# Performance work log

Hardware: AMD Instinct MI355X
Metric: run time of the kernel (lower is better)

The kernel has to match this reference:

```python
import jax, jax.numpy as jnp
import numpy as np

N_NODES = 100000
N_EDGES = 1200000
IN_FEATS = 64
OUT_FEATS = 64


def setup_inputs() -> dict:
    key = jax.random.key(0)
    k1, k2, k3, k4 = jax.random.split(key, 4)
    feature = jax.random.normal(k1, (N_NODES, IN_FEATS), dtype=jnp.float32)
    edge_src = jax.random.randint(k2, (N_EDGES,), 0, N_NODES, dtype=jnp.int32)
    edge_dst = jax.random.randint(k3, (N_EDGES,), 0, N_NODES, dtype=jnp.int32)
    # xavier_normal_ init for linear weight (fan_in=fan_out=64)
    std = float(np.sqrt(2.0 / (IN_FEATS + OUT_FEATS)))
    W = jax.random.normal(k4, (OUT_FEATS, IN_FEATS), dtype=jnp.float32) * std
    b = jnp.zeros((OUT_FEATS,), dtype=jnp.float32)
    return {"feature": feature, "edge_src": edge_src, "edge_dst": edge_dst, "W": W, "b": b}


def reference(feature, edge_src, edge_dst, W, b):
    # copy_src: gather source-node features per edge, then mean-reduce by dst.
    msgs = feature[edge_src]                                   # [E, d_in]
    summed = jax.ops.segment_sum(msgs, edge_dst, num_segments=N_NODES)  # [N, d_in]
    deg = jax.ops.segment_sum(jnp.ones((edge_src.shape[0],), feature.dtype),
                              edge_dst, num_segments=N_NODES)  # [N]
    h = summed / jnp.maximum(deg, 1.0)[:, None]                # mean; 0 for isolated nodes
    # apply_nodes: linear + activation
    h = jnp.einsum("nd,od->no", h, W) + b
    return jax.nn.relu(h)
```

## Files before the change

### kernel.cpp

```cpp
#include <hip/hip_runtime.h>


typedef __attribute__((ext_vector_type(8))) short short8;
typedef __attribute__((ext_vector_type(4))) float floatx4;

constexpr int kNodes = 100000;
constexpr int kEdges = 1200000;

constexpr int kBuckets = 2048;
constexpr int kBucketNodes = 49;

constexpr int kBinBlocks = 256;
constexpr int kEdgesPerBlock = 4688;
constexpr int kEPT = (kEdgesPerBlock + 1023) / 1024;

constexpr int kCap = 1024;
constexpr float kFxScale = 262144.0f;
constexpr int kAccStride = 68;

constexpr int kWsFeat   = 0;
constexpr int kWsOff    = 3200000;
constexpr int kWsBinned = kWsOff + (kBuckets + 1) * kBinBlocks;

__device__ __forceinline__ unsigned bf16rne(float f) {
  unsigned u = __float_as_uint(f);
  return (u + 0x7fffu + ((u >> 16) & 1u)) >> 16;
}

__global__ __launch_bounds__(1024) void gcn_build(
    const float* __restrict__ feat,
    const int* __restrict__ src, const int* __restrict__ dst,
    int* __restrict__ ws) {
  uint4* fb16 = (uint4*)(ws + kWsFeat);
  int* offTT  = ws + kWsOff;
  int* binned = ws + kWsBinned;

  __shared__ int lhist[kBuckets];
  __shared__ int lcur[kBuckets];
  __shared__ int wsum[16];

  const int tid = threadIdx.x;
  lhist[tid] = 0;
  lhist[tid + 1024] = 0;
  __syncthreads();

  const int e0 = blockIdx.x * kEdgesPerBlock;
  const int cnt = min(kEdgesPerBlock, kEdges - e0);
  int es[kEPT], ebk[kEPT], edl[kEPT];
  #pragma unroll
  for (int k = 0; k < kEPT; ++k) {
    const int j = tid + k * 1024;
    if (j < cnt) {
      es[k] = src[e0 + j];
      const int d = dst[e0 + j];
      const int bk = d / kBucketNodes;
      ebk[k] = bk;
      edl[k] = d - bk * kBucketNodes;
      atomicAdd(&lhist[bk], 1);
    }
  }

  const int t = blockIdx.x * 1024 + tid;
  for (int i = t; i < kNodes * 8; i += kBinBlocks * 1024) {
    const float* fr = feat + (size_t)(i >> 3) * 64 + (i & 7);
    uint4 p;
    p.x = bf16rne(fr[0])  | (bf16rne(fr[8])  << 16);
    p.y = bf16rne(fr[16]) | (bf16rne(fr[24]) << 16);
    p.z = bf16rne(fr[32]) | (bf16rne(fr[40]) << 16);
    p.w = bf16rne(fr[48]) | (bf16rne(fr[56]) << 16);
    fb16[i] = p;
  }
  __syncthreads();

  const int a  = lhist[tid * 2];
  const int b2 = lhist[tid * 2 + 1];
  const int own = a + b2;
  const int wv = tid >> 6, ln = tid & 63;
  int sc = own;
  #pragma unroll
  for (int off = 1; off < 64; off <<= 1) {
    const int v = __shfl_up(sc, off, 64);
    if (ln >= off) sc += v;
  }
  if (ln == 63) wsum[wv] = sc;
  __syncthreads();
  if (tid < 64) {
    int tw = (tid < 16) ? wsum[tid] : 0;
    #pragma unroll
    for (int off = 1; off < 16; off <<= 1) {
      const int v = __shfl_up(tw, off, 64);
      if (tid >= off) tw += v;
    }
    if (tid < 16) wsum[tid] = tw;
  }
  __syncthreads();
  const int e0p = sc - own + (wv ? wsum[wv - 1] : 0);
  lcur[tid * 2]     = e0p;
  lcur[tid * 2 + 1] = e0p + a;
  offTT[(tid * 2) * kBinBlocks + blockIdx.x]     = e0p;
  offTT[(tid * 2 + 1) * kBinBlocks + blockIdx.x] = e0p + a;
  if (tid == 0) offTT[kBuckets * kBinBlocks + blockIdx.x] = cnt;
  __syncthreads();

  int* myBin = binned + blockIdx.x * kEdgesPerBlock;
  #pragma unroll
  for (int k = 0; k < kEPT; ++k) {
    const int j = tid + k * 1024;
    if (j < cnt) {
      const int pos = atomicAdd(&lcur[ebk[k]], 1);
      myBin[pos] = es[k] | (edl[k] << 17);
    }
  }
}

__global__ __launch_bounds__(512, 8) void gcn_aggregate(
    const int*   __restrict__ ws_in,
    const float* __restrict__ W,
    const float* __restrict__ b,
    float*       __restrict__ out) {
  const uint4* fb16 = (const uint4*)(ws_in + kWsFeat);
  const int* offTT  = ws_in + kWsOff;
  const int* binned = ws_in + kWsBinned;

  __shared__ __align__(16) char uShared[64 * 72 * 2];
  __shared__ __align__(16) int accum[kBucketNodes * kAccStride];
  __shared__ int    deg[64];
  __shared__ int    sh[64];
  __shared__ int    runL[kBinBlocks + 1];
  __shared__ int    runG[kBinBlocks];
  __shared__ ushort Wb16[64 * 64];
  __shared__ float  bsh[64];
  int*    lsrc  = (int*)uShared;
  ushort* hsAll = (ushort*)uShared;

  const int tid = threadIdx.x;
  const int bkt = blockIdx.x;

  if (tid < 64) { deg[tid] = 0; sh[tid] = 0; bsh[tid] = b[tid]; }
  for (int i = tid; i < 4096; i += 512) Wb16[i] = (ushort)bf16rne(W[i]);
  for (int i = tid; i < kBucketNodes * kAccStride; i += 512) accum[i] = 0;

  if (tid < kBinBlocks) {
    const int o0 = offTT[bkt * kBinBlocks + tid];
    const int o1 = offTT[(bkt + 1) * kBinBlocks + tid];
    runL[tid] = o1 - o0;
    runG[tid] = tid * kEdgesPerBlock + o0;
  }
  __syncthreads();
  if (tid < 64) {
    const int base = tid * 4;
    const int v0 = runL[base], v1 = runL[base + 1];
    const int v2 = runL[base + 2], v3 = runL[base + 3];
    const int p1 = v0 + v1, p2 = p1 + v2, tot = p2 + v3;
    int sc = tot;
    #pragma unroll
    for (int off = 1; off < 64; off <<= 1) {
      const int v = __shfl_up(sc, off, 64);
      if (tid >= off) sc += v;
    }
    const int ex = sc - tot;
    runL[base]     = ex;
    runL[base + 1] = ex + v0;
    runL[base + 2] = ex + p1;
    runL[base + 3] = ex + p2;
    if (tid == 63) runL[kBinBlocks] = sc;
  }
  __syncthreads();

  int sz = runL[kBinBlocks];
  if (sz > kCap) sz = kCap;

  auto mapRead = [&](int j) -> unsigned {
    int lo = 0, hi = kBinBlocks;
    #pragma unroll
    for (int it = 0; it < 8; ++it) {
      const int mid = (lo + hi) >> 1;
      if (runL[mid] <= j) lo = mid; else hi = mid;
    }
    return (unsigned)binned[runG[lo] + (j - runL[lo])];
  };

  const int j0 = tid, j1 = tid + 512;
  const bool va = j0 < sz, vb = j1 < sz;
  unsigned ea = 0, eb = 0;
  if (va) {
    ea = mapRead(j0);
    atomicAdd(&deg[ea >> 17], 1);
    atomicAdd(&sh[(ea & 0x1FFFFu) >> 11], 1);
  }
  if (vb) {
    eb = mapRead(j1);
    atomicAdd(&deg[eb >> 17], 1);
    atomicAdd(&sh[(eb & 0x1FFFFu) >> 11], 1);
  }
  __syncthreads();

  if (tid < 64) {
    const int own = sh[tid];
    int s = own;
    #pragma unroll
    for (int off = 1; off < 64; off <<= 1) {
      const int v = __shfl_up(s, off, 64);
      if (tid >= off) s += v;
    }
    sh[tid] = s - own;
  }
  __syncthreads();

  if (va) { const int p = atomicAdd(&sh[(ea & 0x1FFFFu) >> 11], 1); lsrc[p] = (int)ea; }
  if (vb) { const int p = atomicAdd(&sh[(eb & 0x1FFFFu) >> 11], 1); lsrc[p] = (int)eb; }
  __syncthreads();

  const int wave = tid >> 6;
  const int lane = tid & 63;
  const int g = lane >> 3;
  const int c = lane & 7;
  {
    const int slot = wave * 8 + g;
    #pragma unroll 2
    for (int j = slot; j < sz; j += 64) {
      const unsigned e = (unsigned)lsrc[j];
      const uint4 v = fb16[(size_t)(e & 0x1FFFFu) * 8 + c];
      int* rp = accum + (int)(e >> 17) * kAccStride + c;
      atomicAdd(rp + 0,  (int)(__uint_as_float(v.x << 16)          * kFxScale));
      atomicAdd(rp + 8,  (int)(__uint_as_float(v.x & 0xffff0000u) * kFxScale));
      atomicAdd(rp + 16, (int)(__uint_as_float(v.y << 16)          * kFxScale));
      atomicAdd(rp + 24, (int)(__uint_as_float(v.y & 0xffff0000u) * kFxScale));
      atomicAdd(rp + 32, (int)(__uint_as_float(v.z << 16)          * kFxScale));
      atomicAdd(rp + 40, (int)(__uint_as_float(v.z & 0xffff0000u) * kFxScale));
      atomicAdd(rp + 48, (int)(__uint_as_float(v.w << 16)          * kFxScale));
      atomicAdd(rp + 56, (int)(__uint_as_float(v.w & 0xffff0000u) * kFxScale));
    }
  }
  __syncthreads();

  {
    const int nd = tid >> 3;
    const int ch = tid & 7;
    if (nd < kBucketNodes) {
      const int dg = deg[nd];
      const float inv = 1.0f / (kFxScale * (float)(dg > 1 ? dg : 1));
      const int* arow = accum + nd * kAccStride + ch * 8;
      const int4 pa = *(const int4*)(arow);
      const int4 pb = *(const int4*)(arow + 4);
      unsigned h0 = bf16rne((float)pa.x * inv);
      unsigned h1 = bf16rne((float)pa.y * inv);
      unsigned h2 = bf16rne((float)pa.z * inv);
      unsigned h3 = bf16rne((float)pa.w * inv);
      unsigned h4 = bf16rne((float)pb.x * inv);
      unsigned h5 = bf16rne((float)pb.y * inv);
      unsigned h6 = bf16rne((float)pb.z * inv);
      unsigned h7 = bf16rne((float)pb.w * inv);
      uint4 pk;
      pk.x = h0 | (h1 << 16);
      pk.y = h2 | (h3 << 16);
      pk.z = h4 | (h5 << 16);
      pk.w = h6 | (h7 << 16);
      *(uint4*)(hsAll + nd * 72 + ch * 8) = pk;
    } else {
      *(uint4*)(hsAll + nd * 72 + ch * 8) = make_uint4(0u, 0u, 0u, 0u);
    }
  }
  __syncthreads();

  if (tid < 256) {
    const int w8   = tid >> 6;
    const int ln   = tid & 63;
    const int quad = ln >> 4;
    const int col  = ln & 15;
    const int n0 = bkt * kBucketNodes;

    const short8 af0 = *reinterpret_cast<const short8*>(
        hsAll + (w8 * 16 + col) * 72 + 0 * 32 + quad * 8);
    const short8 af1 = *reinterpret_cast<const short8*>(
        hsAll + (w8 * 16 + col) * 72 + 1 * 32 + quad * 8);

    #pragma unroll
    for (int ob = 0; ob < 4; ++ob) {
      const short8 bf0 = *reinterpret_cast<const short8*>(
          Wb16 + (ob * 16 + col) * 64 + 0 * 32 + quad * 8);
      const short8 bf1 = *reinterpret_cast<const short8*>(
          Wb16 + (ob * 16 + col) * 64 + 1 * 32 + quad * 8);
      floatx4 acc = {0.f, 0.f, 0.f, 0.f};
      acc = __builtin_amdgcn_mfma_f32_16x16x32_bf16(af0, bf0, acc, 0, 0, 0);
      acc = __builtin_amdgcn_mfma_f32_16x16x32_bf16(af1, bf1, acc, 0, 0, 0);

      const int o = ob * 16 + col;
      const float bo = bsh[o];
      #pragma unroll
      for (int r = 0; r < 4; ++r) {
        const int local = w8 * 16 + quad * 4 + r;
        const int node = n0 + local;
        if (local < kBucketNodes && node < kNodes) {
          const float v = acc[r] + bo;
          out[(size_t)node * 64 + o] = v > 0.0f ? v : 0.0f;
        }
      }
    }
  }
}

extern "C" void kernel_launch(void* const* d_in, const int* in_sizes, int n_in,
                              void* d_out, int out_size, void* d_ws, size_t ws_size,
                              hipStream_t stream) {
  const float* feature  = (const float*)d_in[0];
  const int*   edge_src = (const int*)  d_in[1];
  const int*   edge_dst = (const int*)  d_in[2];
  const float* W        = (const float*)d_in[3];
  const float* b        = (const float*)d_in[4];

  float* out = (float*)d_out;
  int*   ws  = (int*)d_ws;

  gcn_build<<<kBinBlocks, 1024, 0, stream>>>(feature, edge_src, edge_dst, ws);
  gcn_aggregate<<<kBuckets, 512, 0, stream>>>(ws, W, b, out);
}
```

Baseline: 131.4 us.

## Replace two-level binned edge sort with global atomic bucket append

Drops the per-block histogram, scan and offset table. Each edge now claims a slot in its fixed-capacity bucket region through a global atomicAdd, and the W-to-bf16 conversion moves into a small prep kernel that also zeroes the counters. The aggregate kernel reads its bucket's edges directly instead of binary-searching 256 runs, and reads W and b from global memory instead of staging them in shared memory. In exchange it adds global atomic contention on 2048 counters and lowers the per-bucket cap to 768, so any edges past the cap are silently dropped.

New measurement: 261.9 us. +99.2%, slower.

```diff
diff --git a/kernel.cpp b/kernel.cpp
--- a/kernel.cpp
+++ b/kernel.cpp
@@ -10,58 +10,42 @@
 constexpr int kBuckets = 2048;
 constexpr int kBucketNodes = 49;
 
-constexpr int kBinBlocks = 256;
-constexpr int kEdgesPerBlock = 4688;
-constexpr int kEPT = (kEdgesPerBlock + 1023) / 1024;
-
-constexpr int kCap = 1024;
+constexpr int kCap = 768;
 constexpr float kFxScale = 262144.0f;
 constexpr int kAccStride = 68;
 
 constexpr int kWsFeat   = 0;
-constexpr int kWsOff    = 3200000;
-constexpr int kWsBinned = kWsOff + (kBuckets + 1) * kBinBlocks;
+constexpr int kWsCnt    = 3200000;
+constexpr int kWsWb     = 3202048;
+constexpr int kWsSorted = 3204096;
 
 __device__ __forceinline__ unsigned bf16rne(float f) {
   unsigned u = __float_as_uint(f);
   return (u + 0x7fffu + ((u >> 16) & 1u)) >> 16;
 }
 
-__global__ __launch_bounds__(1024) void gcn_build(
+__global__ __launch_bounds__(512) void gcn_prep(
+    const float* __restrict__ W, int* __restrict__ ws) {
+  int* gcnt = ws + kWsCnt;
+  ushort* Wb16g = (ushort*)(ws + kWsWb);
+  const int t = blockIdx.x * 512 + threadIdx.x;
+  gcnt[t] = 0;
+  Wb16g[t]        = (ushort)bf16rne(W[t]);
+  Wb16g[t + 2048] = (ushort)bf16rne(W[t + 2048]);
+}
+
+__global__ __launch_bounds__(256) void gcn_build(
     const float* __restrict__ feat,
     const int* __restrict__ src, const int* __restrict__ dst,
     int* __restrict__ ws) {
-  uint4* fb16 = (uint4*)(ws + kWsFeat);
-  int* offTT  = ws + kWsOff;
-  int* binned = ws + kWsBinned;
-
-  __shared__ int lhist[kBuckets];
-  __shared__ int lcur[kBuckets];
-  __shared__ int wsum[16];
-
-  const int tid = threadIdx.x;
-  lhist[tid] = 0;
-  lhist[tid + 1024] = 0;
-  __syncthreads();
-
-  const int e0 = blockIdx.x * kEdgesPerBlock;
-  const int cnt = min(kEdgesPerBlock, kEdges - e0);
-  int es[kEPT], ebk[kEPT], edl[kEPT];
-  #pragma unroll
-  for (int k = 0; k < kEPT; ++k) {
-    const int j = tid + k * 1024;
-    if (j < cnt) {
-      es[k] = src[e0 + j];
-      const int d = dst[e0 + j];
-      const int bk = d / kBucketNodes;
-      ebk[k] = bk;
-      edl[k] = d - bk * kBucketNodes;
-      atomicAdd(&lhist[bk], 1);
-    }
-  }
-
-  const int t = blockIdx.x * 1024 + tid;
-  for (int i = t; i < kNodes * 8; i += kBinBlocks * 1024) {
+  uint4* fb16  = (uint4*)(ws + kWsFeat);
+  int* gcnt    = ws + kWsCnt;
+  int* gsorted = ws + kWsSorted;
+
+  const int t = blockIdx.x * 256 + threadIdx.x;
+  const int stride = gridDim.x * 256;
+
+  for (int i = t; i < kNodes * 8; i += stride) {
     const float* fr = feat + (size_t)(i >> 3) * 64 + (i & 7);
     uint4 p;
     p.x = bf16rne(fr[0])  | (bf16rne(fr[8])  << 16);
@@ -70,126 +54,53 @@
     p.w = bf16rne(fr[48]) | (bf16rne(fr[56]) << 16);
     fb16[i] = p;
   }
-  __syncthreads();
-
-  const int a  = lhist[tid * 2];
-  const int b2 = lhist[tid * 2 + 1];
-  const int own = a + b2;
-  const int wv = tid >> 6, ln = tid & 63;
-  int sc = own;
-  #pragma unroll
-  for (int off = 1; off < 64; off <<= 1) {
-    const int v = __shfl_up(sc, off, 64);
-    if (ln >= off) sc += v;
-  }
-  if (ln == 63) wsum[wv] = sc;
-  __syncthreads();
-  if (tid < 64) {
-    int tw = (tid < 16) ? wsum[tid] : 0;
-    #pragma unroll
-    for (int off = 1; off < 16; off <<= 1) {
-      const int v = __shfl_up(tw, off, 64);
-      if (tid >= off) tw += v;
-    }
-    if (tid < 16) wsum[tid] = tw;
-  }
-  __syncthreads();
-  const int e0p = sc - own + (wv ? wsum[wv - 1] : 0);
-  lcur[tid * 2]     = e0p;
-  lcur[tid * 2 + 1] = e0p + a;
-  offTT[(tid * 2) * kBinBlocks + blockIdx.x]     = e0p;
-  offTT[(tid * 2 + 1) * kBinBlocks + blockIdx.x] = e0p + a;
-  if (tid == 0) offTT[kBuckets * kBinBlocks + blockIdx.x] = cnt;
-  __syncthreads();
-
-  int* myBin = binned + blockIdx.x * kEdgesPerBlock;
-  #pragma unroll
-  for (int k = 0; k < kEPT; ++k) {
-    const int j = tid + k * 1024;
-    if (j < cnt) {
-      const int pos = atomicAdd(&lcur[ebk[k]], 1);
-      myBin[pos] = es[k] | (edl[k] << 17);
-    }
+
+  for (int e = t; e < kEdges; e += stride) {
+    const int s = src[e];
+    const int d = dst[e];
+    const int bk = d / kBucketNodes;
+    const int dL = d - bk * kBucketNodes;
+    const int pos = atomicAdd(&gcnt[bk], 1);
+    if (pos < kCap) gsorted[bk * kCap + pos] = s | (dL << 17);
   }
 }
 
 __global__ __launch_bounds__(512, 8) void gcn_aggregate(
     const int*   __restrict__ ws_in,
-    const float* __restrict__ W,
     const float* __restrict__ b,
     float*       __restrict__ out) {
-  const uint4* fb16 = (const uint4*)(ws_in + kWsFeat);
-  const int* offTT  = ws_in + kWsOff;
-  const int* binned = ws_in + kWsBinned;
+  const uint4* fb16    = (const uint4*)(ws_in + kWsFeat);
+  const int* gcnt      = ws_in + kWsCnt;
+  const ushort* Wb16g  = (const ushort*)(ws_in + kWsWb);
+  const int* gsorted   = ws_in + kWsSorted;
 
   __shared__ __align__(16) char uShared[64 * 72 * 2];
   __shared__ __align__(16) int accum[kBucketNodes * kAccStride];
-  __shared__ int    deg[64];
-  __shared__ int    sh[64];
-  __shared__ int    runL[kBinBlocks + 1];
-  __shared__ int    runG[kBinBlocks];
-  __shared__ ushort Wb16[64 * 64];
-  __shared__ float  bsh[64];
+  __shared__ int deg[64];
+  __shared__ int sh[64];
   int*    lsrc  = (int*)uShared;
   ushort* hsAll = (ushort*)uShared;
 
   const int tid = threadIdx.x;
   const int bkt = blockIdx.x;
 
-  if (tid < 64) { deg[tid] = 0; sh[tid] = 0; bsh[tid] = b[tid]; }
-  for (int i = tid; i < 4096; i += 512) Wb16[i] = (ushort)bf16rne(W[i]);
+  if (tid < 64) { deg[tid] = 0; sh[tid] = 0; }
   for (int i = tid; i < kBucketNodes * kAccStride; i += 512) accum[i] = 0;
 
-  if (tid < kBinBlocks) {
-    const int o0 = offTT[bkt * kBinBlocks + tid];
-    const int o1 = offTT[(bkt + 1) * kBinBlocks + tid];
-    runL[tid] = o1 - o0;
-    runG[tid] = tid * kEdgesPerBlock + o0;
-  }
-  __syncthreads();
-  if (tid < 64) {
-    const int base = tid * 4;
-    const int v0 = runL[base], v1 = runL[base + 1];
-    const int v2 = runL[base + 2], v3 = runL[base + 3];
-    const int p1 = v0 + v1, p2 = p1 + v2, tot = p2 + v3;
-    int sc = tot;
-    #pragma unroll
-    for (int off = 1; off < 64; off <<= 1) {
-      const int v = __shfl_up(sc, off, 64);
-      if (tid >= off) sc += v;
-    }
-    const int ex = sc - tot;
-    runL[base]     = ex;
-    runL[base + 1] = ex + v0;
-    runL[base + 2] = ex + p1;
-    runL[base + 3] = ex + p2;
-    if (tid == 63) runL[kBinBlocks] = sc;
-  }
-  __syncthreads();
-
-  int sz = runL[kBinBlocks];
+  int sz = gcnt[bkt];
   if (sz > kCap) sz = kCap;
-
-  auto mapRead = [&](int j) -> unsigned {
-    int lo = 0, hi = kBinBlocks;
-    #pragma unroll
-    for (int it = 0; it < 8; ++it) {
-      const int mid = (lo + hi) >> 1;
-      if (runL[mid] <= j) lo = mid; else hi = mid;
-    }
-    return (unsigned)binned[runG[lo] + (j - runL[lo])];
-  };
+  const int ebase = bkt * kCap;
 
   const int j0 = tid, j1 = tid + 512;
   const bool va = j0 < sz, vb = j1 < sz;
   unsigned ea = 0, eb = 0;
   if (va) {
-    ea = mapRead(j0);
+    ea = (unsigned)gsorted[ebase + j0];
     atomicAdd(&deg[ea >> 17], 1);
     atomicAdd(&sh[(ea & 0x1FFFFu) >> 11], 1);
   }
   if (vb) {
-    eb = mapRead(j1);
+    eb = (unsigned)gsorted[ebase + j1];
     atomicAdd(&deg[eb >> 17], 1);
     atomicAdd(&sh[(eb & 0x1FFFFu) >> 11], 1);
   }
@@ -278,15 +189,15 @@
     #pragma unroll
     for (int ob = 0; ob < 4; ++ob) {
       const short8 bf0 = *reinterpret_cast<const short8*>(
-          Wb16 + (ob * 16 + col) * 64 + 0 * 32 + quad * 8);
+          Wb16g + (ob * 16 + col) * 64 + 0 * 32 + quad * 8);
       const short8 bf1 = *reinterpret_cast<const short8*>(
-          Wb16 + (ob * 16 + col) * 64 + 1 * 32 + quad * 8);
+          Wb16g + (ob * 16 + col) * 64 + 1 * 32 + quad * 8);
       floatx4 acc = {0.f, 0.f, 0.f, 0.f};
       acc = __builtin_amdgcn_mfma_f32_16x16x32_bf16(af0, bf0, acc, 0, 0, 0);
       acc = __builtin_amdgcn_mfma_f32_16x16x32_bf16(af1, bf1, acc, 0, 0, 0);
 
       const int o = ob * 16 + col;
-      const float bo = bsh[o];
+      const float bo = b[o];
       #pragma unroll
       for (int r = 0; r < 4; ++r) {
         const int local = w8 * 16 + quad * 4 + r;
@@ -312,6 +223,7 @@
   float* out = (float*)d_out;
   int*   ws  = (int*)d_ws;
 
-  gcn_build<<<kBinBlocks, 1024, 0, stream>>>(feature, edge_src, edge_dst, ws);
-  gcn_aggregate<<<kBuckets, 512, 0, stream>>>(ws, W, b, out);
-}
+  gcn_prep<<<4, 512, 0, stream>>>(W, ws);
+  gcn_build<<<1024, 256, 0, stream>>>(feature, edge_src, edge_dst, ws);
+  gcn_aggregate<<<kBuckets, 512, 0, stream>>>(ws, b, out);
+}
```
